# Kernel tuning notes

Hardware: AMD Instinct MI355X
Metric: run time of the kernel (lower is better)

Reference implementation:

```python
import jax, jax.numpy as jnp
import numpy as np

NUM_HEADS = 12
NUM_PATCHES = 4096
DIM = 768
IN_DIMS = DIM // NUM_HEADS
SCALE = NUM_PATCHES ** (-0.5)
LN_EPS = 1e-5


def setup_inputs() -> dict:
    key = jax.random.key(0)
    ks = jax.random.split(key, 14)
    s = 0.02
    return {
        "x": jax.random.normal(ks[0], (16, NUM_PATCHES, DIM), dtype=jnp.float32),
        "wq": jax.random.normal(ks[1], (DIM, DIM), dtype=jnp.float32) * s,
        "bq": jnp.zeros((DIM,), dtype=jnp.float32),
        "wk": jax.random.normal(ks[2], (DIM, DIM), dtype=jnp.float32) * s,
        "bk": jnp.zeros((DIM,), dtype=jnp.float32),
        "w_g": jax.random.normal(ks[3], (NUM_PATCHES,), dtype=jnp.float32),
        "w_fc": jax.random.normal(ks[4], (IN_DIMS, DIM), dtype=jnp.float32) * s,
        "b_fc": jnp.zeros((DIM,), dtype=jnp.float32),
        "w_fc2": jax.random.normal(ks[5], (NUM_HEADS, NUM_HEADS), dtype=jnp.float32) * s,
        "b_fc2": jnp.zeros((NUM_HEADS,), dtype=jnp.float32),
        "w_proj": jax.random.normal(ks[6], (DIM, DIM), dtype=jnp.float32) * s,
        "b_proj": jnp.zeros((DIM,), dtype=jnp.float32),
        "gamma": jnp.ones((DIM,), dtype=jnp.float32),
        "beta": jnp.zeros((DIM,), dtype=jnp.float32),
    }


def layernorm(x, gamma, beta):
    mu = jnp.mean(x, axis=-1, keepdims=True)
    var = jnp.mean(jnp.square(x - mu), axis=-1, keepdims=True)
    return (x - mu) * jax.lax.rsqrt(var + LN_EPS) * gamma + beta


def reference(x, wq, bq, wk, bk, w_g, w_fc, b_fc, w_fc2, b_fc2, w_proj, b_proj, gamma, beta):
    bs, n, d = x.shape
    q = x @ wq + bq                      # (b,n,d)  fc_q
    k = x @ wk + bk                      # (b,n,d)  fc_k (reassigned x in torch)
    # query_weight = (q^T @ w_g)^T -> (b,1,d); softmax over channel dim
    qw = jnp.einsum("bnd,n->bd", q, w_g) * SCALE
    A = jax.nn.softmax(qw, axis=-1)      # (b,d)
    # G = sum_n(A * k): A is constant over n, so equals A * sum_n k
    G = A * jnp.sum(k, axis=1)           # (b,d)
    # sigmoid gating chain on pooled q
    dv = jnp.mean(q, axis=1)             # (b,d)   AdaptiveAvgPool over n
    dv = dv.reshape(bs, NUM_HEADS, IN_DIMS)
    dv = jax.nn.gelu(dv @ w_fc + b_fc, approximate=False)   # (b,H,d)
    dv = dv.reshape(bs, d, NUM_HEADS)    # reshape (not transpose), as in torch
    dv = dv @ w_fc2 + b_fc2              # (b,d,H)
    dv = jax.nn.sigmoid(jnp.mean(dv, axis=-1))               # (b,d)
    G = G * dv                           # (b,d)
    out = (G[:, None, :] * k) @ w_proj + b_proj + layernorm(k, gamma, beta)
    return out
```

## Files before the change

kernel.cpp:

```cpp
#include <hip/hip_runtime.h>
#include <hip/hip_bf16.h>
#include <math.h>

#define NB 16
#define NP 4096
#define DDIM 768
#define MTOT (NB*NP)
#define SCALEF 0.015625f
#define LNEPS 1e-5f

typedef __attribute__((ext_vector_type(8))) short bf16x8;
typedef __attribute__((ext_vector_type(4))) float f32x4;
typedef __attribute__((ext_vector_type(4))) unsigned int u32x4;
typedef unsigned short us;

__device__ __forceinline__ us f2b(float f){
  union { float f; unsigned int u; } v; v.f = f;
  unsigned int u = v.u;
  unsigned int r = (u + 0x7FFFu + ((u >> 16) & 1u)) >> 16;
  return (us)r;
}
__device__ __forceinline__ unsigned int pack2(float a, float b){
  return (unsigned int)f2b(a) | ((unsigned int)f2b(b) << 16);
}
__device__ __forceinline__ float b2f(us h){
  union { unsigned int u; float f; } v; v.u = ((unsigned int)h) << 16;
  return v.f;
}
__device__ __forceinline__ float b2f_lo(unsigned int u){
  union { unsigned int x; float f; } v; v.x = u << 16; return v.f;
}
__device__ __forceinline__ float b2f_hi(unsigned int u){
  union { unsigned int x; float f; } v; v.x = u & 0xFFFF0000u; return v.f;
}

typedef __attribute__((address_space(1))) const unsigned int gas_u32;
typedef __attribute__((address_space(3))) unsigned int las_u32;
__device__ __forceinline__ void gl2lds16(const void* g, void* l){
  __builtin_amdgcn_global_load_lds((gas_u32*)g, (las_u32*)l, 16, 0, 0);
}

__global__ __launch_bounds__(384) void convert_x(const float* __restrict__ x,
                                                 const float* __restrict__ w_g,
                                                 us* __restrict__ xb,
                                                 float* __restrict__ xwp,
                                                 float* __restrict__ xsp){
  __shared__ float sw[4][DDIM], ss[4][DDIM];
  int blk = blockIdx.x, t = threadIdx.x;
  int c = t % 96, g = t / 96;
  int cg = c * 8;
  int r0 = blk * 128;
  float accw[8] = {0,0,0,0,0,0,0,0}, accs[8] = {0,0,0,0,0,0,0,0};
  for (int r = g; r < 128; r += 4){
    int row = r0 + r;
    float wg = w_g[row & (NP - 1)];
    const float4* s = reinterpret_cast<const float4*>(x + (size_t)row * DDIM + cg);
    float4 a = s[0], b = s[1];
    u32x4 w;
    w[0] = pack2(a.x, a.y); w[1] = pack2(a.z, a.w);
    w[2] = pack2(b.x, b.y); w[3] = pack2(b.z, b.w);
    *reinterpret_cast<u32x4*>(xb + (size_t)row * DDIM + cg) = w;
    float v[8] = {a.x, a.y, a.z, a.w, b.x, b.y, b.z, b.w};
    #pragma unroll
    for (int j = 0; j < 8; ++j){ accs[j] += v[j]; accw[j] += wg * v[j]; }
  }
  #pragma unroll
  for (int j = 0; j < 8; ++j){ sw[g][cg + j] = accw[j]; ss[g][cg + j] = accs[j]; }
  __syncthreads();
  if (g == 0){
    int b = r0 >> 12, mc = (r0 & (NP - 1)) >> 7;
    size_t base = ((size_t)b * 32 + mc) * DDIM;
    #pragma unroll
    for (int j = 0; j < 8; ++j){
      xwp[base + cg + j] = accw[j] + sw[1][cg + j] + sw[2][cg + j] + sw[3][cg + j];
      xsp[base + cg + j] = accs[j] + ss[1][cg + j] + ss[2][cg + j] + ss[3][cg + j];
    }
  }
}

__global__ __launch_bounds__(256) void prep_w(const float* __restrict__ wk,
                                              const float* __restrict__ wp,
                                              us* __restrict__ wtk,
                                              us* __restrict__ wt2){
  int idx = blockIdx.x * 256 + threadIdx.x;
  const int tot = DDIM * DDIM;
  if (idx < tot){
    int n = idx / DDIM, k = idx % DDIM;
    wtk[idx] = f2b(wk[k * DDIM + n]);
  }
  int i2 = idx - tot;
  if (i2 >= 0 && i2 < tot){
    int n = i2 / DDIM, k = i2 % DDIM;
    wt2[i2] = f2b(wp[k * DDIM + n]);
  }
}

__global__ __launch_bounds__(256) void xmv(const float* __restrict__ xwp,
                                           const float* __restrict__ xsp,
                                           const float* __restrict__ wq,
                                           const float* __restrict__ wk,
                                           float* __restrict__ qwv,
                                           float* __restrict__ qmv,
                                           float* __restrict__ ksv){
  __shared__ float sxw[DDIM], sxs[DDIM];
  __shared__ float pa[2][128], pb_[2][128], pc[2][128];
  int blk = blockIdx.x;
  int b = blk / 6, dc = (blk % 6) * 128;
  int t = threadIdx.x;
  for (int col = t; col < DDIM; col += 256){
    float s0 = 0.f, s1 = 0.f;
    for (int mc = 0; mc < 32; ++mc){
      size_t base = ((size_t)b * 32 + mc) * DDIM + col;
      s0 += xwp[base]; s1 += xsp[base];
    }
    sxw[col] = s0; sxs[col] = s1;
  }
  __syncthreads();
  int d = dc + (t & 127), h = t >> 7;
  float aq = 0.f, am = 0.f, ak = 0.f;
  for (int k = h * 384; k < h * 384 + 384; ++k){
    float w1 = wq[(size_t)k * DDIM + d];
    float w2 = wk[(size_t)k * DDIM + d];
    float xw = sxw[k], xs = sxs[k];
    aq += xw * w1; am += xs * w1; ak += xs * w2;
  }
  pa[h][t & 127] = aq; pb_[h][t & 127] = am; pc[h][t & 127] = ak;
  __syncthreads();
  if (h == 0){
    size_t o = (size_t)b * DDIM + d;
    qwv[o] = aq + pa[1][t];
    qmv[o] = am + pb_[1][t];
    ksv[o] = ak + pc[1][t];
  }
}

__global__ __launch_bounds__(256) void ln_reduce(const float* __restrict__ lnS,
                                                 const float* __restrict__ lnQ,
                                                 float2* __restrict__ rstats){
  int r = blockIdx.x * 256 + threadIdx.x;
  float s = lnS[r] + lnS[MTOT + r] + lnS[2*MTOT + r];
  float q = lnQ[r] + lnQ[MTOT + r] + lnQ[2*MTOT + r];
  float mu = s * (1.0f / DDIM);
  float var = q * (1.0f / DDIM) - mu * mu;
  rstats[r] = make_float2(mu, rsqrtf(var + LNEPS));
}

__device__ __forceinline__ void gemm256_core(const us* __restrict__ Ag,
                                             const us* __restrict__ Bg,
                                             us* lds, int t,
                                             f32x4 (&acc)[4][4][2]){
  us* ldsA = lds;
  us* ldsB = lds + 32768;
  const int wave = t >> 6, lane = t & 63;
  const int wr = wave >> 2, wc = wave & 3, lr = lane & 15, lh = lane >> 4;
  const int srow = t >> 3;
  const int scell = (t & 7) ^ ((t >> 3) & 7);
  const int key8 = lane & 7;

  auto stage_all = [&](int kt){
    int pb = (kt & 1) << 14;
    #pragma unroll
    for (int j = 0; j < 4; ++j){
      const us* sa = Ag + (size_t)(j*64 + srow) * DDIM + kt*64 + scell*8;
      gl2lds16(sa, ldsA + pb + j*4096 + (wave << 9));
    }
    #pragma unroll
    for (int j = 0; j < 4; ++j){
      const us* sb = Bg + (size_t)(j*64 + srow) * DDIM + kt*64 + scell*8;
      gl2lds16(sb, ldsB + pb + j*4096 + (wave << 9));
    }
  };

  stage_all(0);

  bf16x8 av[4][2], bv0[2][2], bv1[2][2];

  for (int kt = 0; kt < 12; ++kt){
    asm volatile("s_waitcnt vmcnt(0)" ::: "memory");
    __builtin_amdgcn_s_barrier();
    __builtin_amdgcn_sched_barrier(0);
    if (kt < 11) stage_all(kt + 1);

    const int pb = (kt & 1) << 14;
    const us* Ab = ldsA + pb;
    const us* Bb = ldsB + pb;

    #pragma unroll
    for (int fm = 0; fm < 4; ++fm){
      int ra = 0*128 + wr*64 + fm*16 + lr;
      #pragma unroll
      for (int kk = 0; kk < 2; ++kk)
        av[fm][kk] = *reinterpret_cast<const bf16x8*>(
            &Ab[ra*64 + ((((kk<<2)|lh) ^ key8) << 3)]);
    }
    #pragma unroll
    for (int fn = 0; fn < 2; ++fn){
      int rb0 = 0*128 + wc*32 + fn*16 + lr;
      int rb1 = 1*128 + wc*32 + fn*16 + lr;
      #pragma unroll
      for (int kk = 0; kk < 2; ++kk){
        bv0[fn][kk] = *reinterpret_cast<const bf16x8*>(
            &Bb[rb0*64 + ((((kk<<2)|lh) ^ key8) << 3)]);
        bv1[fn][kk] = *reinterpret_cast<const bf16x8*>(
            &Bb[rb1*64 + ((((kk<<2)|lh) ^ key8) << 3)]);
      }
    }
    #pragma unroll
    for (int fm = 0; fm < 4; ++fm)
      #pragma unroll
      for (int fn = 0; fn < 2; ++fn)
        #pragma unroll
        for (int kk = 0; kk < 2; ++kk){
          acc[0][fm][fn] = __builtin_amdgcn_mfma_f32_16x16x32_bf16(
              bv0[fn][kk], av[fm][kk], acc[0][fm][fn], 0, 0, 0);
          acc[1][fm][fn] = __builtin_amdgcn_mfma_f32_16x16x32_bf16(
              bv1[fn][kk], av[fm][kk], acc[1][fm][fn], 0, 0, 0);
        }

    #pragma unroll
    for (int fm = 0; fm < 4; ++fm){
      int ra = 1*128 + wr*64 + fm*16 + lr;
      #pragma unroll
      for (int kk = 0; kk < 2; ++kk)
        av[fm][kk] = *reinterpret_cast<const bf16x8*>(
            &Ab[ra*64 + ((((kk<<2)|lh) ^ key8) << 3)]);
    }
    #pragma unroll
    for (int fm = 0; fm < 4; ++fm)
      #pragma unroll
      for (int fn = 0; fn < 2; ++fn)
        #pragma unroll
        for (int kk = 0; kk < 2; ++kk){
          acc[2][fm][fn] = __builtin_amdgcn_mfma_f32_16x16x32_bf16(
              bv0[fn][kk], av[fm][kk], acc[2][fm][fn], 0, 0, 0);
          acc[3][fm][fn] = __builtin_amdgcn_mfma_f32_16x16x32_bf16(
              bv1[fn][kk], av[fm][kk], acc[3][fm][fn], 0, 0, 0);
        }
  }
  __builtin_amdgcn_s_barrier();
}

__global__ __launch_bounds__(512, 2) void gemm_k(
    const us* __restrict__ xb, const us* __restrict__ wtk,
    const float* __restrict__ bk,
    us* __restrict__ kout,
    float* __restrict__ lnS, float* __restrict__ lnQ)
{
  extern __shared__ us lds[];
  int bid = blockIdx.x;
  int swz = (bid & 7) * ((int)gridDim.x >> 3) + (bid >> 3);
  int bn = swz % 3, bm = swz / 3;
  int m0 = bm * 256, n0 = bn * 256;
  int t = threadIdx.x;

  f32x4 acc[4][4][2] = {};
  gemm256_core(xb + (size_t)m0 * DDIM, wtk + (size_t)n0 * DDIM, lds, t, acc);

  int wave = t >> 6, lane = t & 63;
  int wr = wave >> 2, wc = wave & 3, lr = lane & 15, lh = lane >> 4;

  float4 bias4[2][2];
  #pragma unroll
  for (int qn = 0; qn < 2; ++qn)
    #pragma unroll
    for (int fn = 0; fn < 2; ++fn){
      int col = qn*128 + wc*32 + fn*16 + lh*4;
      bias4[qn][fn] = *reinterpret_cast<const float4*>(&bk[n0 + col]);
    }

  #pragma unroll
  for (int p = 0; p < 4; ++p){
    int qm = p >> 1, qn = p & 1;
    #pragma unroll
    for (int fm = 0; fm < 4; ++fm){
      int row = qm*128 + wr*64 + fm*16 + lr;
      #pragma unroll
      for (int fn = 0; fn < 2; ++fn){
        int col = qn*128 + wc*32 + fn*16 + lh*4;
        uint2 w;
        w.x = pack2(acc[p][fm][fn][0] + bias4[qn][fn].x,
                    acc[p][fm][fn][1] + bias4[qn][fn].y);
        w.y = pack2(acc[p][fm][fn][2] + bias4[qn][fn].z,
                    acc[p][fm][fn][3] + bias4[qn][fn].w);
        *reinterpret_cast<uint2*>(&lds[row*256 + (col ^ ((row & 7) << 3))]) = w;
      }
    }
  }
  __syncthreads();

  int c8 = t & 31, rb = t >> 5;
  float rs16[16], rq16[16];
  #pragma unroll
  for (int s = 0; s < 16; ++s){
    int row = s*16 + rb;
    u32x4 ch = *reinterpret_cast<const u32x4*>(&lds[row*256 + ((c8 ^ (row & 7)) << 3)]);
    *reinterpret_cast<u32x4*>(kout + (size_t)(m0+row)*DDIM + n0 + c8*8) = ch;
    float ss = 0.f, qq = 0.f;
    #pragma unroll
    for (int i = 0; i < 4; ++i){
      float v0 = b2f_lo(ch[i]), v1 = b2f_hi(ch[i]);
      ss += v0 + v1; qq += v0*v0 + v1*v1;
    }
    rs16[s] = ss; rq16[s] = qq;
  }
  __syncthreads();
  float* rowP = reinterpret_cast<float*>(lds);
  float* rowQ = rowP + 8192;
  #pragma unroll
  for (int s = 0; s < 16; ++s){
    int row = s*16 + rb;
    rowP[row*32 + c8] = rs16[s];
    rowQ[row*32 + c8] = rq16[s];
  }
  __syncthreads();
  if (t < 256){
    float rs_ = 0.f, rq_ = 0.f;
    #pragma unroll
    for (int i = 0; i < 32; ++i){ rs_ += rowP[t*32 + i]; rq_ += rowQ[t*32 + i]; }
    lnS[(size_t)bn * MTOT + m0 + t] = rs_;
    lnQ[(size_t)bn * MTOT + m0 + t] = rq_;
  }
}

__global__ __launch_bounds__(256) void prep_wb(const us* __restrict__ wt2,
                                               const float* __restrict__ g,
                                               us* __restrict__ wbuf){
  size_t idx = (size_t)blockIdx.x * 256 + threadIdx.x;
  int d = (int)(idx % DDIM);
  size_t nd = idx / DDIM;
  int n = (int)(nd % DDIM);
  int b = (int)(nd / DDIM);
  float v = b2f(wt2[n * DDIM + d]) * g[(size_t)b * DDIM + d];
  wbuf[idx] = f2b(v);
}

__global__ __launch_bounds__(256) void combine(
    const float* __restrict__ qwv, const float* __restrict__ qmv,
    const float* __restrict__ ksv,
    const float* __restrict__ bq, const float* __restrict__ bk,
    const float* __restrict__ w_g,
    const float* __restrict__ w_fc, const float* __restrict__ b_fc,
    const float* __restrict__ w_fc2, const float* __restrict__ b_fc2,
    float* __restrict__ g)
{
  __shared__ float smA[DDIM];
  __shared__ float smQM[DDIM];
  __shared__ float smKS[DDIM];
  __shared__ float tmat[12][DDIM];
  __shared__ float red[256];
  __shared__ float wbar[12];
  __shared__ float bbar;
  int b = blockIdx.x, t = threadIdx.x;

  float sw = 0.f;
  for (int i = t; i < NP; i += 256) sw += w_g[i];
  red[t] = sw; __syncthreads();
  for (int off = 128; off; off >>= 1){
    if (t < off) red[t] += red[t + off];
    __syncthreads();
  }
  float sumwg = red[0];
  __syncthreads();

  for (int col = t; col < DDIM; col += 256){
    size_t o = (size_t)b * DDIM + col;
    smA[col]  = (qwv[o] + bq[col] * sumwg) * SCALEF;
    smQM[col] = qmv[o] * (1.0f / NP) + bq[col];
    smKS[col] = ksv[o] + (float)NP * bk[col];
  }
  __syncthreads();

  float lmax = -1e30f;
  for (int col = t; col < DDIM; col += 256) lmax = fmaxf(lmax, smA[col]);
  red[t] = lmax; __syncthreads();
  for (int off = 128; off; off >>= 1){
    if (t < off) red[t] = fmaxf(red[t], red[t + off]);
    __syncthreads();
  }
  float mx = red[0];
  __syncthreads();
  float lsum = 0.f;
  for (int col = t; col < DDIM; col += 256){
    float e = __expf(smA[col] - mx);
    smA[col] = e; lsum += e;
  }
  red[t] = lsum; __syncthreads();
  for (int off = 128; off; off >>= 1){
    if (t < off) red[t] += red[t + off];
    __syncthreads();
  }
  float inv = 1.0f / red[0];
  for (int col = t; col < DDIM; col += 256) smA[col] *= inv;

  if (t < 12){
    float s = 0.f;
    for (int j = 0; j < 12; ++j) s += w_fc2[t * 12 + j];
    wbar[t] = s * (1.0f / 12.0f);
  }
  if (t == 12){
    float s = 0.f;
    for (int j = 0; j < 12; ++j) s += b_fc2[j];
    bbar = s * (1.0f / 12.0f);
  }
  __syncthreads();
  for (int idx = t; idx < 12 * DDIM; idx += 256){
    int h = idx / DDIM, j = idx % DDIM;
    float s = b_fc[j];
    const float* qm = &smQM[h * 64];
    #pragma unroll 4
    for (int i = 0; i < 64; ++i) s += qm[i] * w_fc[i * DDIM + j];
    tmat[h][j] = 0.5f * s * (1.0f + erff(s * 0.70710678118654752f));
  }
  __syncthreads();
  for (int p = t; p < DDIM; p += 256){
    float s = bbar;
    #pragma unroll
    for (int m = 0; m < 12; ++m){
      int f = p * 12 + m;
      s += tmat[f / DDIM][f % DDIM] * wbar[m];
    }
    float dv = 1.0f / (1.0f + __expf(-s));
    g[(size_t)b * DDIM + p] = smA[p] * smKS[p] * dv;
  }
}

__global__ __launch_bounds__(512, 2) void gemm_out(
    const us* __restrict__ kin, const us* __restrict__ wbuf,
    const float2* __restrict__ rstats,
    const float* __restrict__ bp, const float* __restrict__ gamma,
    const float* __restrict__ beta,
    float* __restrict__ out)
{
  extern __shared__ us lds[];
  int bid = blockIdx.x;
  int swz = (bid & 7) * ((int)gridDim.x >> 3) + (bid >> 3);
  int bn = swz % 3, bm = swz / 3;
  int m0 = bm * 256, n0 = bn * 256;
  int t = threadIdx.x;
  int b = m0 >> 12;

  f32x4 acc[4][4][2] = {};
  gemm256_core(kin + (size_t)m0 * DDIM,
               wbuf + (size_t)b * DDIM * DDIM + (size_t)n0 * DDIM, lds, t, acc);

  int wave = t >> 6, lane = t & 63;
  int wr = wave >> 2, wc = wave & 3, lr = lane & 15, lh = lane >> 4;

  #pragma unroll
  for (int j = 0; j < 16; ++j){
    int row = j*16 + (t >> 5);
    const us* src = kin + (size_t)(m0 + row) * DDIM + n0 + (((t & 31) ^ (row & 7)) << 3);
    gl2lds16(src, lds + j*4096 + (wave << 9));
  }
  float2 st2[2][4];
  #pragma unroll
  for (int qm = 0; qm < 2; ++qm)
    #pragma unroll
    for (int fm = 0; fm < 4; ++fm)
      st2[qm][fm] = rstats[m0 + qm*128 + wr*64 + fm*16 + lr];
  asm volatile("s_waitcnt vmcnt(0)" ::: "memory");
  __syncthreads();

  #pragma unroll
  for (int p = 0; p < 4; ++p){
    int qm = p >> 1, qn = p & 1;
    #pragma unroll
    for (int fn = 0; fn < 2; ++fn){
      int col = qn*128 + wc*32 + fn*16 + lh*4;
      float4 bpv = *reinterpret_cast<const float4*>(&bp[n0 + col]);
      float4 gmv = *reinterpret_cast<const float4*>(&gamma[n0 + col]);
      float4 btv = *reinterpret_cast<const float4*>(&beta[n0 + col]);
      #pragma unroll
      for (int fm = 0; fm < 4; ++fm){
        int row = qm*128 + wr*64 + fm*16 + lr;
        uint2 kw = *reinterpret_cast<const uint2*>(&lds[row*256 + (col ^ ((row & 7) << 3))]);
        float2 st = st2[qm][fm];
        acc[p][fm][fn][0] += bpv.x + (b2f_lo(kw.x) - st.x) * st.y * gmv.x + btv.x;
        acc[p][fm][fn][1] += bpv.y + (b2f_hi(kw.x) - st.x) * st.y * gmv.y + btv.y;
        acc[p][fm][fn][2] += bpv.z + (b2f_lo(kw.y) - st.x) * st.y * gmv.z + btv.z;
        acc[p][fm][fn][3] += bpv.w + (b2f_hi(kw.y) - st.x) * st.y * gmv.w + btv.w;
      }
    }
  }
  __syncthreads();

  float* fb = reinterpret_cast<float*>(lds);
  #pragma unroll
  for (int h = 0; h < 2; ++h){
    #pragma unroll
    for (int qm2 = 0; qm2 < 2; ++qm2){
      int p = qm2*2 + h;
      #pragma unroll
      for (int fm = 0; fm < 4; ++fm){
        int row = qm2*128 + wr*64 + fm*16 + lr;
        #pragma unroll
        for (int fn = 0; fn < 2; ++fn){
          int c = wc*32 + fn*16 + lh*4;
          *reinterpret_cast<f32x4*>(&fb[row*128 + (c ^ ((row & 7) << 2))]) = acc[p][fm][fn];
        }
      }
    }
    __syncthreads();
    #pragma unroll
    for (int s = 0; s < 16; ++s){
      int u = s*512 + t;
      int row = u >> 5, c4 = u & 31;
      float4 vv = *reinterpret_cast<const float4*>(&fb[row*128 + ((c4 ^ (row & 7)) << 2)]);
      *reinterpret_cast<float4*>(&out[(size_t)(m0 + row) * DDIM + n0 + h*128 + c4*4]) = vv;
    }
    __syncthreads();
  }
}

extern "C" void kernel_launch(void* const* d_in, const int* in_sizes, int n_in,
                              void* d_out, int out_size, void* d_ws, size_t ws_size,
                              hipStream_t stream)
{
  const float* x      = (const float*)d_in[0];
  const float* wq     = (const float*)d_in[1];
  const float* bq     = (const float*)d_in[2];
  const float* wk     = (const float*)d_in[3];
  const float* bk     = (const float*)d_in[4];
  const float* w_g    = (const float*)d_in[5];
  const float* w_fc   = (const float*)d_in[6];
  const float* b_fc   = (const float*)d_in[7];
  const float* w_fc2  = (const float*)d_in[8];
  const float* b_fc2  = (const float*)d_in[9];
  const float* w_proj = (const float*)d_in[10];
  const float* b_proj = (const float*)d_in[11];
  const float* gamma  = (const float*)d_in[12];
  const float* beta   = (const float*)d_in[13];
  float* out = (float*)d_out;

  char* ws = (char*)d_ws;
  us*     xb    = (us*)(ws);
  us*     kbuf  = (us*)(ws + 100663296);
  us*     wtk   = (us*)(ws + 201326592);
  us*     wt2   = (us*)(ws + 202506240);
  us*     wbuf  = (us*)(ws + 203685888);
  float*  xwp   = (float*)(ws + 222560256);
  float*  xsp   = (float*)(ws + 224133120);
  float*  lnS   = (float*)(ws + 225705984);
  float*  lnQ   = (float*)(ws + 226492416);
  float*  g     = (float*)(ws + 227278848);
  float2* rstat = (float2*)(ws + 227328000);
  float*  qwv   = (float*)(ws + 227852288);
  float*  qmv   = (float*)(ws + 227901440);
  float*  ksv   = (float*)(ws + 227950592);

  convert_x<<<dim3(MTOT / 128), dim3(384), 0, stream>>>(x, w_g, xb, xwp, xsp);
  prep_w<<<dim3(2 * DDIM * DDIM / 256), dim3(256), 0, stream>>>(wk, w_proj, wtk, wt2);
  xmv<<<dim3(NB * 6), dim3(256), 0, stream>>>(xwp, xsp, wq, wk, qwv, qmv, ksv);
  gemm_k<<<dim3((MTOT / 256) * 3), dim3(512), 131072, stream>>>(
      xb, wtk, bk, kbuf, lnS, lnQ);
  ln_reduce<<<dim3(MTOT / 256), dim3(256), 0, stream>>>(lnS, lnQ, rstat);
  combine<<<dim3(NB), dim3(256), 0, stream>>>(
      qwv, qmv, ksv, bq, bk, w_g, w_fc, b_fc, w_fc2, b_fc2, g);
  prep_wb<<<dim3(NB * DDIM * DDIM / 256), dim3(256), 0, stream>>>(wt2, g, wbuf);
  gemm_out<<<dim3((MTOT / 256) * 3), dim3(512), 131072, stream>>>(
      kbuf, wbuf, rstat, b_proj, gamma, beta, out);
}
```

Before: 473.3 us.

## Shrink GEMM tiles to 128x128 with triple-buffered LDS pipeline

Both GEMMs move from 256x256 tiles (512 threads, each wave holding a 4x4x2 accumulator) to 128x128 tiles with a three-stage LDS ring and partial vmcnt waits, so two k-slices are in flight at once. The gemm_out epilogue now reads k directly from global memory and writes fp32 output straight from registers instead of staging through LDS. LayerNorm partial sums grow from 3 to 6 column blocks per row. Smaller tiles cut register pressure and improve the pipelining and load balance, at the cost of more global and L2 traffic for operands and uncoalesced direct stores. Launch bounds drop from 2 to 1 blocks per CU, and 96KB of LDS per block likely still limits occupancy.

```diff
diff --git a/kernel.cpp b/kernel.cpp
--- a/kernel.cpp
+++ b/kernel.cpp
@@ -138,109 +138,76 @@
                                                  const float* __restrict__ lnQ,
                                                  float2* __restrict__ rstats){
   int r = blockIdx.x * 256 + threadIdx.x;
-  float s = lnS[r] + lnS[MTOT + r] + lnS[2*MTOT + r];
-  float q = lnQ[r] + lnQ[MTOT + r] + lnQ[2*MTOT + r];
+  float s = 0.f, q = 0.f;
+  #pragma unroll
+  for (int kb = 0; kb < 6; ++kb){
+    s += lnS[(size_t)kb * MTOT + r];
+    q += lnQ[(size_t)kb * MTOT + r];
+  }
   float mu = s * (1.0f / DDIM);
   float var = q * (1.0f / DDIM) - mu * mu;
   rstats[r] = make_float2(mu, rsqrtf(var + LNEPS));
 }
 
-__device__ __forceinline__ void gemm256_core(const us* __restrict__ Ag,
-                                             const us* __restrict__ Bg,
-                                             us* lds, int t,
-                                             f32x4 (&acc)[4][4][2]){
+__device__ __forceinline__ void gemm128_r3(const us* __restrict__ Ag,
+                                           const us* __restrict__ Bg,
+                                           us* lds, int t,
+                                           f32x4 (&acc)[4][2]){
   us* ldsA = lds;
-  us* ldsB = lds + 32768;
-  const int wave = t >> 6, lane = t & 63;
-  const int wr = wave >> 2, wc = wave & 3, lr = lane & 15, lh = lane >> 4;
+  us* ldsB = lds + 24576;
+  const int lane = t & 63, wave = t >> 6;
+  const int wr = wave >> 2, wc = wave & 3;
+  const int lr = lane & 15, lh = lane >> 4;
+  const int key8 = lane & 7;
   const int srow = t >> 3;
-  const int scell = (t & 7) ^ ((t >> 3) & 7);
-  const int key8 = lane & 7;
-
-  auto stage_all = [&](int kt){
-    int pb = (kt & 1) << 14;
-    #pragma unroll
-    for (int j = 0; j < 4; ++j){
-      const us* sa = Ag + (size_t)(j*64 + srow) * DDIM + kt*64 + scell*8;
-      gl2lds16(sa, ldsA + pb + j*4096 + (wave << 9));
-    }
-    #pragma unroll
-    for (int j = 0; j < 4; ++j){
-      const us* sb = Bg + (size_t)(j*64 + srow) * DDIM + kt*64 + scell*8;
-      gl2lds16(sb, ldsB + pb + j*4096 + (wave << 9));
+  const int scell = (t & 7) ^ (srow & 7);
+
+  auto stage = [&](int kt){
+    int sb = (kt % 3) * 8192;
+    int ko = kt * 64;
+    #pragma unroll
+    for (int j = 0; j < 2; ++j){
+      gl2lds16(Ag + (size_t)(j*64 + srow) * DDIM + ko + scell*8,
+               ldsA + sb + j*4096 + t*8);
+      gl2lds16(Bg + (size_t)(j*64 + srow) * DDIM + ko + scell*8,
+               ldsB + sb + j*4096 + t*8);
     }
   };
 
-  stage_all(0);
-
-  bf16x8 av[4][2], bv0[2][2], bv1[2][2];
-
+  stage(0); stage(1);
+
+  #pragma unroll
   for (int kt = 0; kt < 12; ++kt){
-    asm volatile("s_waitcnt vmcnt(0)" ::: "memory");
+    if (kt < 11) { asm volatile("s_waitcnt vmcnt(4)" ::: "memory"); }
+    else         { asm volatile("s_waitcnt vmcnt(0)" ::: "memory"); }
+    __builtin_amdgcn_sched_barrier(0);
     __builtin_amdgcn_s_barrier();
-    __builtin_amdgcn_sched_barrier(0);
-    if (kt < 11) stage_all(kt + 1);
-
-    const int pb = (kt & 1) << 14;
-    const us* Ab = ldsA + pb;
-    const us* Bb = ldsB + pb;
-
-    #pragma unroll
-    for (int fm = 0; fm < 4; ++fm){
-      int ra = 0*128 + wr*64 + fm*16 + lr;
+    if (kt < 10) stage(kt + 2);
+    const us* Ab = ldsA + (kt % 3) * 8192;
+    const us* Bb = ldsB + (kt % 3) * 8192;
+    bf16x8 av[4], bv[2];
+    #pragma unroll
+    for (int kk = 0; kk < 2; ++kk){
       #pragma unroll
-      for (int kk = 0; kk < 2; ++kk)
-        av[fm][kk] = *reinterpret_cast<const bf16x8*>(
-            &Ab[ra*64 + ((((kk<<2)|lh) ^ key8) << 3)]);
-    }
-    #pragma unroll
-    for (int fn = 0; fn < 2; ++fn){
-      int rb0 = 0*128 + wc*32 + fn*16 + lr;
-      int rb1 = 1*128 + wc*32 + fn*16 + lr;
-      #pragma unroll
-      for (int kk = 0; kk < 2; ++kk){
-        bv0[fn][kk] = *reinterpret_cast<const bf16x8*>(
-            &Bb[rb0*64 + ((((kk<<2)|lh) ^ key8) << 3)]);
-        bv1[fn][kk] = *reinterpret_cast<const bf16x8*>(
-            &Bb[rb1*64 + ((((kk<<2)|lh) ^ key8) << 3)]);
-      }
-    }
-    #pragma unroll
-    for (int fm = 0; fm < 4; ++fm)
+      for (int fm = 0; fm < 4; ++fm)
+        av[fm] = *reinterpret_cast<const bf16x8*>(
+            &Ab[(wr*64 + fm*16 + lr)*64 + ((((kk<<2)|lh) ^ key8) << 3)]);
       #pragma unroll
       for (int fn = 0; fn < 2; ++fn)
+        bv[fn] = *reinterpret_cast<const bf16x8*>(
+            &Bb[(wc*32 + fn*16 + lr)*64 + ((((kk<<2)|lh) ^ key8) << 3)]);
+      #pragma unroll
+      for (int fm = 0; fm < 4; ++fm)
         #pragma unroll
-        for (int kk = 0; kk < 2; ++kk){
-          acc[0][fm][fn] = __builtin_amdgcn_mfma_f32_16x16x32_bf16(
-              bv0[fn][kk], av[fm][kk], acc[0][fm][fn], 0, 0, 0);
-          acc[1][fm][fn] = __builtin_amdgcn_mfma_f32_16x16x32_bf16(
-              bv1[fn][kk], av[fm][kk], acc[1][fm][fn], 0, 0, 0);
-        }
-
-    #pragma unroll
-    for (int fm = 0; fm < 4; ++fm){
-      int ra = 1*128 + wr*64 + fm*16 + lr;
-      #pragma unroll
-      for (int kk = 0; kk < 2; ++kk)
-        av[fm][kk] = *reinterpret_cast<const bf16x8*>(
-            &Ab[ra*64 + ((((kk<<2)|lh) ^ key8) << 3)]);
-    }
-    #pragma unroll
-    for (int fm = 0; fm < 4; ++fm)
-      #pragma unroll
-      for (int fn = 0; fn < 2; ++fn)
-        #pragma unroll
-        for (int kk = 0; kk < 2; ++kk){
-          acc[2][fm][fn] = __builtin_amdgcn_mfma_f32_16x16x32_bf16(
-              bv0[fn][kk], av[fm][kk], acc[2][fm][fn], 0, 0, 0);
-          acc[3][fm][fn] = __builtin_amdgcn_mfma_f32_16x16x32_bf16(
-              bv1[fn][kk], av[fm][kk], acc[3][fm][fn], 0, 0, 0);
-        }
+        for (int fn = 0; fn < 2; ++fn)
+          acc[fm][fn] = __builtin_amdgcn_mfma_f32_16x16x32_bf16(
+              bv[fn], av[fm], acc[fm][fn], 0, 0, 0);
+    }
   }
   __builtin_amdgcn_s_barrier();
 }
 
-__global__ __launch_bounds__(512, 2) void gemm_k(
+__global__ __launch_bounds__(512, 1) void gemm_k(
     const us* __restrict__ xb, const us* __restrict__ wtk,
     const float* __restrict__ bk,
     us* __restrict__ kout,
@@ -249,51 +216,43 @@
   extern __shared__ us lds[];
   int bid = blockIdx.x;
   int swz = (bid & 7) * ((int)gridDim.x >> 3) + (bid >> 3);
-  int bn = swz % 3, bm = swz / 3;
-  int m0 = bm * 256, n0 = bn * 256;
+  int bn = swz % 6, bm = swz / 6;
+  int m0 = bm * 128, n0 = bn * 128;
   int t = threadIdx.x;
 
-  f32x4 acc[4][4][2] = {};
-  gemm256_core(xb + (size_t)m0 * DDIM, wtk + (size_t)n0 * DDIM, lds, t, acc);
-
-  int wave = t >> 6, lane = t & 63;
+  f32x4 acc[4][2] = {};
+  gemm128_r3(xb + (size_t)m0 * DDIM, wtk + (size_t)n0 * DDIM, lds, t, acc);
+
+  int lane = t & 63, wave = t >> 6;
   int wr = wave >> 2, wc = wave & 3, lr = lane & 15, lh = lane >> 4;
 
-  float4 bias4[2][2];
-  #pragma unroll
-  for (int qn = 0; qn < 2; ++qn)
+  float4 bias4[2];
+  #pragma unroll
+  for (int fn = 0; fn < 2; ++fn){
+    int col = wc*32 + fn*16 + lh*4;
+    bias4[fn] = *reinterpret_cast<const float4*>(&bk[n0 + col]);
+  }
+
+  #pragma unroll
+  for (int fm = 0; fm < 4; ++fm){
+    int row = wr*64 + fm*16 + lr;
     #pragma unroll
     for (int fn = 0; fn < 2; ++fn){
-      int col = qn*128 + wc*32 + fn*16 + lh*4;
-      bias4[qn][fn] = *reinterpret_cast<const float4*>(&bk[n0 + col]);
-    }
-
-  #pragma unroll
-  for (int p = 0; p < 4; ++p){
-    int qm = p >> 1, qn = p & 1;
-    #pragma unroll
-    for (int fm = 0; fm < 4; ++fm){
-      int row = qm*128 + wr*64 + fm*16 + lr;
-      #pragma unroll
-      for (int fn = 0; fn < 2; ++fn){
-        int col = qn*128 + wc*32 + fn*16 + lh*4;
-        uint2 w;
-        w.x = pack2(acc[p][fm][fn][0] + bias4[qn][fn].x,
-                    acc[p][fm][fn][1] + bias4[qn][fn].y);
-        w.y = pack2(acc[p][fm][fn][2] + bias4[qn][fn].z,
-                    acc[p][fm][fn][3] + bias4[qn][fn].w);
-        *reinterpret_cast<uint2*>(&lds[row*256 + (col ^ ((row & 7) << 3))]) = w;
-      }
-    }
-  }
-  __syncthreads();
-
-  int c8 = t & 31, rb = t >> 5;
-  float rs16[16], rq16[16];
-  #pragma unroll
-  for (int s = 0; s < 16; ++s){
-    int row = s*16 + rb;
-    u32x4 ch = *reinterpret_cast<const u32x4*>(&lds[row*256 + ((c8 ^ (row & 7)) << 3)]);
+      int col = wc*32 + fn*16 + lh*4;
+      uint2 w;
+      w.x = pack2(acc[fm][fn][0] + bias4[fn].x, acc[fm][fn][1] + bias4[fn].y);
+      w.y = pack2(acc[fm][fn][2] + bias4[fn].z, acc[fm][fn][3] + bias4[fn].w);
+      *reinterpret_cast<uint2*>(&lds[row*128 + (col ^ ((row & 7) << 3))]) = w;
+    }
+  }
+  __syncthreads();
+
+  int c8 = t & 15, rb = t >> 4;
+  float rs4[4], rq4[4];
+  #pragma unroll
+  for (int s = 0; s < 4; ++s){
+    int row = s*32 + rb;
+    u32x4 ch = *reinterpret_cast<const u32x4*>(&lds[row*128 + ((c8 ^ (row & 7)) << 3)]);
     *reinterpret_cast<u32x4*>(kout + (size_t)(m0+row)*DDIM + n0 + c8*8) = ch;
     float ss = 0.f, qq = 0.f;
     #pragma unroll
@@ -301,22 +260,22 @@
       float v0 = b2f_lo(ch[i]), v1 = b2f_hi(ch[i]);
       ss += v0 + v1; qq += v0*v0 + v1*v1;
     }
-    rs16[s] = ss; rq16[s] = qq;
+    rs4[s] = ss; rq4[s] = qq;
   }
   __syncthreads();
   float* rowP = reinterpret_cast<float*>(lds);
-  float* rowQ = rowP + 8192;
-  #pragma unroll
-  for (int s = 0; s < 16; ++s){
-    int row = s*16 + rb;
-    rowP[row*32 + c8] = rs16[s];
-    rowQ[row*32 + c8] = rq16[s];
-  }
-  __syncthreads();
-  if (t < 256){
+  float* rowQ = rowP + 2048;
+  #pragma unroll
+  for (int s = 0; s < 4; ++s){
+    int row = s*32 + rb;
+    rowP[row*16 + c8] = rs4[s];
+    rowQ[row*16 + c8] = rq4[s];
+  }
+  __syncthreads();
+  if (t < 128){
     float rs_ = 0.f, rq_ = 0.f;
     #pragma unroll
-    for (int i = 0; i < 32; ++i){ rs_ += rowP[t*32 + i]; rq_ += rowQ[t*32 + i]; }
+    for (int i = 0; i < 16; ++i){ rs_ += rowP[t*16 + i]; rq_ += rowQ[t*16 + i]; }
     lnS[(size_t)bn * MTOT + m0 + t] = rs_;
     lnQ[(size_t)bn * MTOT + m0 + t] = rq_;
   }
@@ -424,7 +383,7 @@
   }
 }
 
-__global__ __launch_bounds__(512, 2) void gemm_out(
+__global__ __launch_bounds__(512, 1) void gemm_out(
     const us* __restrict__ kin, const us* __restrict__ wbuf,
     const float2* __restrict__ rstats,
     const float* __restrict__ bp, const float* __restrict__ gamma,
@@ -434,81 +393,42 @@
   extern __shared__ us lds[];
   int bid = blockIdx.x;
   int swz = (bid & 7) * ((int)gridDim.x >> 3) + (bid >> 3);
-  int bn = swz % 3, bm = swz / 3;
-  int m0 = bm * 256, n0 = bn * 256;
+  int bn = swz % 6, bm = swz / 6;
+  int m0 = bm * 128, n0 = bn * 128;
   int t = threadIdx.x;
   int b = m0 >> 12;
 
-  f32x4 acc[4][4][2] = {};
-  gemm256_core(kin + (size_t)m0 * DDIM,
-               wbuf + (size_t)b * DDIM * DDIM + (size_t)n0 * DDIM, lds, t, acc);
-
-  int wave = t >> 6, lane = t & 63;
+  f32x4 acc[4][2] = {};
+  gemm128_r3(kin + (size_t)m0 * DDIM,
+             wbuf + (size_t)b * DDIM * DDIM + (size_t)n0 * DDIM, lds, t, acc);
+
+  int lane = t & 63, wave = t >> 6;
   int wr = wave >> 2, wc = wave & 3, lr = lane & 15, lh = lane >> 4;
 
-  #pragma unroll
-  for (int j = 0; j < 16; ++j){
-    int row = j*16 + (t >> 5);
-    const us* src = kin + (size_t)(m0 + row) * DDIM + n0 + (((t & 31) ^ (row & 7)) << 3);
-    gl2lds16(src, lds + j*4096 + (wave << 9));
-  }
-  float2 st2[2][4];
-  #pragma unroll
-  for (int qm = 0; qm < 2; ++qm)
-    #pragma unroll
-    for (int fm = 0; fm < 4; ++fm)
-      st2[qm][fm] = rstats[m0 + qm*128 + wr*64 + fm*16 + lr];
-  asm volatile("s_waitcnt vmcnt(0)" ::: "memory");
-  __syncthreads();
-
-  #pragma unroll
-  for (int p = 0; p < 4; ++p){
-    int qm = p >> 1, qn = p & 1;
-    #pragma unroll
-    for (int fn = 0; fn < 2; ++fn){
-      int col = qn*128 + wc*32 + fn*16 + lh*4;
-      float4 bpv = *reinterpret_cast<const float4*>(&bp[n0 + col]);
-      float4 gmv = *reinterpret_cast<const float4*>(&gamma[n0 + col]);
-      float4 btv = *reinterpret_cast<const float4*>(&beta[n0 + col]);
-      #pragma unroll
-      for (int fm = 0; fm < 4; ++fm){
-        int row = qm*128 + wr*64 + fm*16 + lr;
-        uint2 kw = *reinterpret_cast<const uint2*>(&lds[row*256 + (col ^ ((row & 7) << 3))]);
-        float2 st = st2[qm][fm];
-        acc[p][fm][fn][0] += bpv.x + (b2f_lo(kw.x) - st.x) * st.y * gmv.x + btv.x;
-        acc[p][fm][fn][1] += bpv.y + (b2f_hi(kw.x) - st.x) * st.y * gmv.y + btv.y;
-        acc[p][fm][fn][2] += bpv.z + (b2f_lo(kw.y) - st.x) * st.y * gmv.z + btv.z;
-        acc[p][fm][fn][3] += bpv.w + (b2f_hi(kw.y) - st.x) * st.y * gmv.w + btv.w;
-      }
-    }
-  }
-  __syncthreads();
-
-  float* fb = reinterpret_cast<float*>(lds);
-  #pragma unroll
-  for (int h = 0; h < 2; ++h){
-    #pragma unroll
-    for (int qm2 = 0; qm2 < 2; ++qm2){
-      int p = qm2*2 + h;
-      #pragma unroll
-      for (int fm = 0; fm < 4; ++fm){
-        int row = qm2*128 + wr*64 + fm*16 + lr;
-        #pragma unroll
-        for (int fn = 0; fn < 2; ++fn){
-          int c = wc*32 + fn*16 + lh*4;
-          *reinterpret_cast<f32x4*>(&fb[row*128 + (c ^ ((row & 7) << 2))]) = acc[p][fm][fn];
-        }
-      }
-    }
-    __syncthreads();
-    #pragma unroll
-    for (int s = 0; s < 16; ++s){
-      int u = s*512 + t;
-      int row = u >> 5, c4 = u & 31;
-      float4 vv = *reinterpret_cast<const float4*>(&fb[row*128 + ((c4 ^ (row & 7)) << 2)]);
-      *reinterpret_cast<float4*>(&out[(size_t)(m0 + row) * DDIM + n0 + h*128 + c4*4]) = vv;
-    }
-    __syncthreads();
+  float2 st2[4];
+  #pragma unroll
+  for (int fm = 0; fm < 4; ++fm)
+    st2[fm] = rstats[m0 + wr*64 + fm*16 + lr];
+
+  #pragma unroll
+  for (int fn = 0; fn < 2; ++fn){
+    int col = wc*32 + fn*16 + lh*4;
+    float4 bpv = *reinterpret_cast<const float4*>(&bp[n0 + col]);
+    float4 gmv = *reinterpret_cast<const float4*>(&gamma[n0 + col]);
+    float4 btv = *reinterpret_cast<const float4*>(&beta[n0 + col]);
+    #pragma unroll
+    for (int fm = 0; fm < 4; ++fm){
+      int row = wr*64 + fm*16 + lr;
+      size_t gbase = (size_t)(m0 + row) * DDIM + n0 + col;
+      uint2 kw = *reinterpret_cast<const uint2*>(&kin[gbase]);
+      float2 st = st2[fm];
+      float4 o;
+      o.x = acc[fm][fn][0] + bpv.x + (b2f_lo(kw.x) - st.x) * st.y * gmv.x + btv.x;
+      o.y = acc[fm][fn][1] + bpv.y + (b2f_hi(kw.x) - st.x) * st.y * gmv.y + btv.y;
+      o.z = acc[fm][fn][2] + bpv.z + (b2f_lo(kw.y) - st.x) * st.y * gmv.z + btv.z;
+      o.w = acc[fm][fn][3] + bpv.w + (b2f_hi(kw.y) - st.x) * st.y * gmv.w + btv.w;
+      *reinterpret_cast<float4*>(&out[gbase]) = o;
+    }
   }
 }
 
@@ -541,22 +461,22 @@
   float*  xwp   = (float*)(ws + 222560256);
   float*  xsp   = (float*)(ws + 224133120);
   float*  lnS   = (float*)(ws + 225705984);
-  float*  lnQ   = (float*)(ws + 226492416);
-  float*  g     = (float*)(ws + 227278848);
-  float2* rstat = (float2*)(ws + 227328000);
-  float*  qwv   = (float*)(ws + 227852288);
-  float*  qmv   = (float*)(ws + 227901440);
-  float*  ksv   = (float*)(ws + 227950592);
+  float*  lnQ   = (float*)(ws + 227278848);
+  float*  g     = (float*)(ws + 228851712);
+  float2* rstat = (float2*)(ws + 228900864);
+  float*  qwv   = (float*)(ws + 229425152);
+  float*  qmv   = (float*)(ws + 229474304);
+  float*  ksv   = (float*)(ws + 229523456);
 
   convert_x<<<dim3(MTOT / 128), dim3(384), 0, stream>>>(x, w_g, xb, xwp, xsp);
   prep_w<<<dim3(2 * DDIM * DDIM / 256), dim3(256), 0, stream>>>(wk, w_proj, wtk, wt2);
   xmv<<<dim3(NB * 6), dim3(256), 0, stream>>>(xwp, xsp, wq, wk, qwv, qmv, ksv);
-  gemm_k<<<dim3((MTOT / 256) * 3), dim3(512), 131072, stream>>>(
+  gemm_k<<<dim3((MTOT / 128) * 6), dim3(512), 98304, stream>>>(
       xb, wtk, bk, kbuf, lnS, lnQ);
   ln_reduce<<<dim3(MTOT / 256), dim3(256), 0, stream>>>(lnS, lnQ, rstat);
   combine<<<dim3(NB), dim3(256), 0, stream>>>(
       qwv, qmv, ksv, bq, bk, w_g, w_fc, b_fc, w_fc2, b_fc2, g);
   prep_wb<<<dim3(NB * DDIM * DDIM / 256), dim3(256), 0, stream>>>(wt2, g, wbuf);
-  gemm_out<<<dim3((MTOT / 256) * 3), dim3(512), 131072, stream>>>(
+  gemm_out<<<dim3((MTOT / 128) * 6), dim3(512), 98304, stream>>>(
       kbuf, wbuf, rstat, b_proj, gamma, beta, out);
 }
```

Measured after the change: 551.9 us. 16.6% more time.
